# Optimization experiments

Measured on AMD Instinct MI355X. Metric: run time of the kernel, lower is better.

## Reference

```python
import jax, jax.numpy as jnp
import numpy as np

B, M, H = 4, 128, 1024      # docs, padded mentions per doc, LUKE-large hidden
NH, L = 16, 1024            # attention heads, seq_len
E = 64                      # padded entities per doc
R = 512                     # entity pairs per doc
EMB, BS, NC = 768, 64, 97   # embed_size, block_size, num_class


def setup_inputs() -> dict:
    key = jax.random.key(0)
    ks = jax.random.split(key, 12)
    inp = {
        "seq_lhs": jax.random.normal(ks[0], (B, L, H), jnp.float32),
        "ent_lhs": jax.random.normal(ks[1], (B, M, H), jnp.float32),
        "ent_to_seq_attn": jax.random.uniform(ks[2], (B, NH, M, L), jnp.float32),
        "entity_id_labels": jax.random.randint(ks[3], (B, M), 0, E),
        "hts": jax.random.randint(ks[4], (B, R, 2), 0, E),
        "Wh": jax.random.normal(ks[5], (2 * H, EMB), jnp.float32) * 0.02,
        "bh": jax.random.normal(ks[6], (EMB,), jnp.float32) * 0.02,
        "Wt": jax.random.normal(ks[7], (2 * H, EMB), jnp.float32) * 0.02,
        "bt": jax.random.normal(ks[8], (EMB,), jnp.float32) * 0.02,
        "Wb": jax.random.normal(ks[9], (EMB * BS, NC), jnp.float32) * 0.02,
        "bb": jax.random.normal(ks[10], (NC,), jnp.float32) * 0.02,
    }
    return inp


def reference(seq_lhs, ent_lhs, ent_to_seq_attn, entity_id_labels, hts,
              Wh, bh, Wt, bt, Wb, bb):
    # ---- mention -> entity pooling (segment logsumexp / segment mean) ----
    # global segment id per mention: doc_i * E + entity_label
    ids = (jnp.arange(B)[:, None] * E + entity_id_labels).reshape(-1)  # [B*M]
    m = ent_lhs.reshape(B * M, H)

    seg_max = jax.ops.segment_max(m, ids, num_segments=B * E)          # [B*E, H]
    seg_max = jnp.where(jnp.isfinite(seg_max), seg_max, 0.0)           # empty -> 0
    sumexp = jax.ops.segment_sum(jnp.exp(m - seg_max[ids]), ids, num_segments=B * E)
    cnt = jax.ops.segment_sum(jnp.ones((B * M,), m.dtype), ids, num_segments=B * E)  # [B*E]
    lse = seg_max + jnp.log(jnp.maximum(sumexp, 1e-30))
    ent_embeds = jnp.where(cnt[:, None] > 0, lse, 0.0).reshape(B, E, H)

    # mean of entity-to-seq attention over mentions of each entity
    a = ent_to_seq_attn.transpose(0, 2, 1, 3).reshape(B * M, NH, L)
    a_sum = jax.ops.segment_sum(a, ids, num_segments=B * E)            # [B*E, NH, L]
    ent_attn = (a_sum / jnp.maximum(cnt, 1.0)[:, None, None]).reshape(B, E, NH, L)

    # ---- gather head/tail entities for each pair ----
    h_idx, t_idx = hts[..., 0], hts[..., 1]                            # [B, R]
    hs = jnp.take_along_axis(ent_embeds, h_idx[..., None], axis=1)     # [B, R, H]
    ts = jnp.take_along_axis(ent_embeds, t_idx[..., None], axis=1)
    h_attn = jnp.take_along_axis(ent_attn, h_idx[..., None, None], axis=1)  # [B, R, NH, L]
    t_attn = jnp.take_along_axis(ent_attn, t_idx[..., None, None], axis=1)

    # ---- attn-weighted relation-context embedding ----
    ht_attn = (h_attn * t_attn).mean(axis=2)                           # [B, R, L]
    ht_attn = ht_attn / (ht_attn.sum(-1, keepdims=True) + 1e-5)
    rel = jnp.einsum('bld,brl->brd', seq_lhs, ht_attn)                 # [B, R, H]

    # ---- extractors + block bilinear classifier ----
    hs = jnp.tanh(jnp.concatenate([hs, rel], -1) @ Wh + bh)            # [B, R, EMB]
    ts = jnp.tanh(jnp.concatenate([ts, rel], -1) @ Wt + bt)
    N, K = B * R, EMB // BS
    b1 = hs.reshape(N, K, BS)
    b2 = ts.reshape(N, K, BS)
    bl = (b1[:, :, :, None] * b2[:, :, None, :]).reshape(N, EMB * BS)  # [N, 49152]
    class_logits = bl @ Wb + bb                                        # [N, NC]
    return class_logits
```

## Files before the change

### kernel.cpp

```cpp
#include <hip/hip_runtime.h>
#include <cmath>

#define B_ 4
#define M_ 128
#define H_ 1024
#define NH_ 16
#define L_ 1024
#define E_ 64
#define R_ 512
#define EMB_ 768
#define BS_ 64
#define NC_ 97
#define NPAIR_ (B_*R_)
#define LC_ 16

typedef _Float16 half8 __attribute__((ext_vector_type(8)));
typedef float f32x4 __attribute__((ext_vector_type(4)));

#define OFF_EAT    0
#define OFF_VH     2097152
#define OFF_PART   0
#define OFF_SEQT   3145728
#define OFF_G      3145728
#define OFF_RELH   5242880
#define OFF_WBT    6291456
#define OFF_ENTH   9437184
#define OFF_SV     9568256
#define OFF_WHT    9570304
#define OFF_WTT    10356736

__device__ __forceinline__ void gload_lds16(const void* g, void* l) {
    __builtin_amdgcn_global_load_lds(
        (const __attribute__((address_space(1))) unsigned int*)g,
        (__attribute__((address_space(3))) unsigned int*)l, 16, 0, 0);
}

__global__ __launch_bounds__(256) void k_ent_pool(const float* __restrict__ ent_lhs,
                                                  const int* __restrict__ labels,
                                                  _Float16* __restrict__ enth) {
    int blk = blockIdx.x;
    int b = blk >> 6, e = blk & 63;
    __shared__ int lbl[M_];
    int t = threadIdx.x;
    if (t < M_) lbl[t] = labels[b*M_ + t];
    __syncthreads();
    const float* src = ent_lhs + (size_t)b * M_ * H_;
    float mx[4], sm[4];
    #pragma unroll
    for (int j = 0; j < 4; ++j) { mx[j] = -INFINITY; sm[j] = 0.f; }
    int cnt = 0;
    for (int m = 0; m < M_; ++m) {
        if (lbl[m] != e) continue;
        ++cnt;
        const float* row = src + m * H_;
        #pragma unroll
        for (int j = 0; j < 4; ++j) {
            float x = row[t + j*256];
            if (x > mx[j]) { sm[j] = sm[j] * __expf(mx[j] - x) + 1.f; mx[j] = x; }
            else           { sm[j] += __expf(x - mx[j]); }
        }
    }
    _Float16* dst = enth + (size_t)blk * H_;
    #pragma unroll
    for (int j = 0; j < 4; ++j)
        dst[t + j*256] = (_Float16)((cnt > 0) ? (mx[j] + __logf(sm[j])) : 0.f);
}

__global__ __launch_bounds__(256) void k_ent_attn(const float* __restrict__ attn,
                                                  const int* __restrict__ labels,
                                                  _Float16* __restrict__ ea_t) {
    int blk = blockIdx.x;
    int b = blk >> 6, e = blk & 63;
    __shared__ int lbl[M_];
    int t = threadIdx.x;
    if (t < M_) lbl[t] = labels[b*M_ + t];
    __syncthreads();
    const float* src = attn + (size_t)b * NH_ * M_ * L_;
    float acc[16][4] = {};
    int cnt = 0;
    for (int m = 0; m < M_; ++m) {
        if (lbl[m] != e) continue;
        ++cnt;
        const float* mp = src + (size_t)m * L_ + t*4;
        #pragma unroll
        for (int nh = 0; nh < 16; ++nh) {
            float4 v = *(const float4*)(mp + (size_t)nh * M_ * L_);
            acc[nh][0] += v.x; acc[nh][1] += v.y; acc[nh][2] += v.z; acc[nh][3] += v.w;
        }
    }
    float inv = 1.f / fmaxf((float)cnt, 1.f);
    _Float16* dst = ea_t + (size_t)blk * L_ * 16;
    #pragma unroll
    for (int j = 0; j < 4; ++j) {
        int l = t*4 + j;
        half8 o0, o1;
        #pragma unroll
        for (int nh = 0; nh < 8; ++nh) { o0[nh] = (_Float16)(acc[nh][j]*inv); o1[nh] = (_Float16)(acc[nh+8][j]*inv); }
        *(half8*)(dst + (size_t)l*16)     = o0;
        *(half8*)(dst + (size_t)l*16 + 8) = o1;
    }
}

__global__ __launch_bounds__(256) void k_ht(const _Float16* __restrict__ ea_t,
                                            const int* __restrict__ hts,
                                            _Float16* __restrict__ vh) {
    int blk = blockIdx.x;
    int b = blk >> 6, lc = blk & 63;
    int l0 = lc * LC_;
    __shared__ _Float16 tile[64*256];
    int t = threadIdx.x;
    {
        int e = t >> 2, part = t & 3;
        const _Float16* src = ea_t + ((size_t)(b*64 + e)*L_ + l0) * 16;
        #pragma unroll
        for (int u = 0; u < 8; ++u) {
            int unit = part*8 + u;
            int l = unit >> 1, nhh = unit & 1;
            half8 v = *(const half8*)(src + l*16 + nhh*8);
            *(half8*)&tile[e*256 + ((l ^ (e & 15))*16) + nhh*8] = v;
        }
    }
    __syncthreads();
    const int* hp = hts + b * R_ * 2;
    #pragma unroll
    for (int pp = 0; pp < 2; ++pp) {
        int p = pp*256 + t;
        int he = hp[p*2], te = hp[p*2 + 1];
        const _Float16* ha = &tile[he*256];
        const _Float16* ta = &tile[te*256];
        float accl[LC_];
        #pragma unroll
        for (int l = 0; l < LC_; ++l) {
            half8 h0 = *(const half8*)&ha[((l ^ (he & 15))*16)];
            half8 h1 = *(const half8*)&ha[((l ^ (he & 15))*16) + 8];
            half8 t0 = *(const half8*)&ta[((l ^ (te & 15))*16)];
            half8 t1 = *(const half8*)&ta[((l ^ (te & 15))*16) + 8];
            float s = 0.f;
            #pragma unroll
            for (int q = 0; q < 8; ++q)
                s += (float)h0[q]*(float)t0[q] + (float)h1[q]*(float)t1[q];
            accl[l] = s;
        }
        half8 o0, o1;
        #pragma unroll
        for (int q = 0; q < 8; ++q) { o0[q] = (_Float16)accl[q]; o1[q] = (_Float16)accl[q+8]; }
        _Float16* dst = vh + (size_t)(b*R_ + p)*L_ + l0;
        *(half8*)dst = o0;
        *(half8*)(dst + 8) = o1;
    }
}

__global__ __launch_bounds__(256) void k_rowsum(const _Float16* __restrict__ vh,
                                                float* __restrict__ s) {
    int row = blockIdx.x*4 + (threadIdx.x >> 6);
    int lane = threadIdx.x & 63;
    const _Float16* r = vh + (size_t)row * L_;
    float acc = 0.f;
    #pragma unroll
    for (int u = 0; u < 2; ++u) {
        half8 v = *(const half8*)(r + (lane + u*64)*8);
        #pragma unroll
        for (int q = 0; q < 8; ++q) acc += (float)v[q];
    }
    #pragma unroll
    for (int off = 32; off > 0; off >>= 1) acc += __shfl_down(acc, off);
    if (lane == 0) s[row] = acc;
}

__global__ __launch_bounds__(256) void k_prep_seqt(const float* __restrict__ seq,
                                                   _Float16* __restrict__ seqT) {
    int l0 = blockIdx.x*64, d0 = blockIdx.y*64, b = blockIdx.z;
    __shared__ _Float16 sl[64*72];
    int t = threadIdx.x;
    int lr = t >> 4, dc = (t & 15)*4;
    #pragma unroll
    for (int u = 0; u < 4; ++u) {
        int l = lr + u*16;
        float4 v = *(const float4*)(seq + ((size_t)(b*L_ + l0 + l))*H_ + d0 + dc);
        sl[l*72 + dc+0] = (_Float16)v.x; sl[l*72 + dc+1] = (_Float16)v.y;
        sl[l*72 + dc+2] = (_Float16)v.z; sl[l*72 + dc+3] = (_Float16)v.w;
    }
    __syncthreads();
    int d = t >> 2, lo = (t & 3)*16;
    half8 o0, o1;
    #pragma unroll
    for (int q = 0; q < 8; ++q) { o0[q] = sl[(lo+q)*72 + d]; o1[q] = sl[(lo+8+q)*72 + d]; }
    _Float16* dst = seqT + ((size_t)(b*H_ + d0 + d))*L_ + l0 + lo;
    *(half8*)dst = o0;
    *(half8*)(dst + 8) = o1;
}

__global__ __launch_bounds__(256) void k_prep_wt(const float* __restrict__ W,
                                                 _Float16* __restrict__ WT) {
    int k0 = blockIdx.x * 64;
    int d0 = blockIdx.y * 64;
    __shared__ float s[64*65];
    int t = threadIdx.x;
    #pragma unroll
    for (int u = 0; u < 16; ++u) {
        int idx = t + u*256; int rr = idx >> 6, cc = idx & 63;
        s[rr*65 + cc] = W[(size_t)(k0+rr)*EMB_ + d0 + cc];
    }
    __syncthreads();
    #pragma unroll
    for (int u = 0; u < 16; ++u) {
        int idx = t + u*256; int dd = idx >> 6, kk = idx & 63;
        WT[(size_t)(d0+dd)*2048 + k0 + kk] = (_Float16)s[kk*65 + dd];
    }
}

__global__ __launch_bounds__(256) void k_prep_wbt(const float* __restrict__ Wb,
                                                  _Float16* __restrict__ Wbt) {
    int kbi = blockIdx.x;
    __shared__ float s[64*97];
    int t = threadIdx.x;
    size_t gbase = (size_t)kbi * 64 * NC_;
    #pragma unroll
    for (int u = 0; u < 25; ++u) {
        int idx = t + u*256;
        if (idx < 64*NC_) s[idx] = Wb[gbase + idx];
    }
    __syncthreads();
    _Float16* dst = Wbt + (size_t)kbi * 8192;
    #pragma unroll
    for (int u = 0; u < 32; ++u) {
        int idx = t + u*256;
        int c = idx >> 6, j = idx & 63;
        float v = (c < NC_) ? s[j*NC_ + c] : 0.f;
        dst[idx] = (_Float16)v;
    }
}

__global__ __launch_bounds__(256) void k_relmm(const _Float16* __restrict__ vh,
                                               const _Float16* __restrict__ seqT,
                                               const float* __restrict__ sv,
                                               _Float16* __restrict__ relh) {
    const int nt = blockIdx.x;
    const int mt = blockIdx.y;
    const int b  = mt >> 2;
    __shared__ _Float16 As[2][128*64];
    __shared__ _Float16 Bs[2][64*64];
    const int t = threadIdx.x;
    const int w = t >> 6, lane = t & 63;
    const int r = lane & 15, g = lane >> 4;
    const int wm = w >> 1, wn = w & 1;
    const int srow = lane >> 3, scol = ((lane & 7) ^ srow) * 8;

    const _Float16* Ab = vh + (size_t)mt*128*1024;
    const _Float16* Bb = seqT + ((size_t)b*1024 + nt*64)*1024;

    #pragma unroll
    for (int cc = 0; cc < 6; ++cc) {
        int c = w*6 + cc;
        if (c < 16) gload_lds16(Ab + (size_t)(c*8 + srow)*1024 + scol, &As[0][c*512]);
        else        gload_lds16(Bb + (size_t)((c-16)*8 + srow)*1024 + scol, &Bs[0][(c-16)*512]);
    }
    f32x4 acc[4][2] = {};
    __syncthreads();

    for (int k = 0; k < 16; ++k) {
        const int cur = k & 1;
        if (k < 15) {
            const int k0 = (k+1)*64;
            #pragma unroll
            for (int cc = 0; cc < 6; ++cc) {
                int c = w*6 + cc;
                if (c < 16) gload_lds16(Ab + (size_t)(c*8 + srow)*1024 + k0 + scol, &As[cur^1][c*512]);
                else        gload_lds16(Bb + (size_t)((c-16)*8 + srow)*1024 + k0 + scol, &Bs[cur^1][(c-16)*512]);
            }
        }
        half8 aF[4][2], bF[2][2];
        #pragma unroll
        for (int mf = 0; mf < 4; ++mf) {
            int row = wm*64 + mf*16 + r;
            aF[mf][0] = *(const half8*)&As[cur][row*64 + ((g ^ (r&7))*8)];
            aF[mf][1] = *(const half8*)&As[cur][row*64 + (((4+g) ^ (r&7))*8)];
        }
        #pragma unroll
        for (int nf = 0; nf < 2; ++nf) {
            int row = wn*32 + nf*16 + r;
            bF[nf][0] = *(const half8*)&Bs[cur][row*64 + ((g ^ (r&7))*8)];
            bF[nf][1] = *(const half8*)&Bs[cur][row*64 + (((4+g) ^ (r&7))*8)];
        }
        #pragma unroll
        for (int mf = 0; mf < 4; ++mf)
            #pragma unroll
            for (int nf = 0; nf < 2; ++nf) {
                acc[mf][nf] = __builtin_amdgcn_mfma_f32_16x16x32_f16(aF[mf][0], bF[nf][0], acc[mf][nf], 0, 0, 0);
                acc[mf][nf] = __builtin_amdgcn_mfma_f32_16x16x32_f16(aF[mf][1], bF[nf][1], acc[mf][nf], 0, 0, 0);
            }
        __syncthreads();
    }
    #pragma unroll
    for (int mf = 0; mf < 4; ++mf) {
        int nb = mt*128 + wm*64 + mf*16 + g*4;
        float invs[4];
        #pragma unroll
        for (int q = 0; q < 4; ++q) invs[q] = 1.f / (sv[nb + q] + 1.6e-4f);
        #pragma unroll
        for (int nf = 0; nf < 2; ++nf) {
            int d = nt*64 + wn*32 + nf*16 + r;
            #pragma unroll
            for (int q = 0; q < 4; ++q)
                relh[(size_t)(nb + q)*1024 + d] = (_Float16)(acc[mf][nf][q] * invs[q]);
        }
    }
}

__global__ __launch_bounds__(256) void k_bigmm(const _Float16* __restrict__ relh,
                                               const _Float16* __restrict__ enth,
                                               const _Float16* __restrict__ WhT,
                                               const _Float16* __restrict__ WtT,
                                               _Float16* __restrict__ G) {
    const int nt = blockIdx.x;
    const int mt = blockIdx.y;
    __shared__ _Float16 As[2][128*64];
    __shared__ _Float16 Bs[2][128*64];
    const int t = threadIdx.x;
    const int w = t >> 6, lane = t & 63;
    const int r = lane & 15, g = lane >> 4;
    const int wm = w >> 1, wn = w & 1;
    const int srow = lane >> 3, scol = ((lane & 7) ^ srow) * 8;

    const _Float16* Ab = (mt < 16) ? (relh + (size_t)mt*128*1024)
                                   : (enth + (size_t)(mt-16)*128*1024);
    const int koff = (mt < 16) ? 1024 : 0;
    const _Float16* Bb = ((nt < 6) ? (WhT + (size_t)nt*128*2048)
                                   : (WtT + (size_t)(nt-6)*128*2048)) + koff;

    #pragma unroll
    for (int cc = 0; cc < 4; ++cc) {
        int c = w*4 + cc;
        gload_lds16(Ab + (size_t)(c*8 + srow)*1024 + scol, &As[0][c*512]);
        gload_lds16(Bb + (size_t)(c*8 + srow)*2048 + scol, &Bs[0][c*512]);
    }
    f32x4 acc[4][4] = {};
    __syncthreads();

    for (int k = 0; k < 16; ++k) {
        const int cur = k & 1;
        if (k < 15) {
            const int k0 = (k+1)*64;
            #pragma unroll
            for (int cc = 0; cc < 4; ++cc) {
                int c = w*4 + cc;
                gload_lds16(Ab + (size_t)(c*8 + srow)*1024 + k0 + scol, &As[cur^1][c*512]);
                gload_lds16(Bb + (size_t)(c*8 + srow)*2048 + k0 + scol, &Bs[cur^1][c*512]);
            }
        }
        half8 aF[4][2], bF[4][2];
        #pragma unroll
        for (int mf = 0; mf < 4; ++mf) {
            int row = wm*64 + mf*16 + r;
            aF[mf][0] = *(const half8*)&As[cur][row*64 + ((g ^ (r&7))*8)];
            aF[mf][1] = *(const half8*)&As[cur][row*64 + (((4+g) ^ (r&7))*8)];
        }
        #pragma unroll
        for (int nf = 0; nf < 4; ++nf) {
            int row = wn*64 + nf*16 + r;
            bF[nf][0] = *(const half8*)&Bs[cur][row*64 + ((g ^ (r&7))*8)];
            bF[nf][1] = *(const half8*)&Bs[cur][row*64 + (((4+g) ^ (r&7))*8)];
        }
        #pragma unroll
        for (int mf = 0; mf < 4; ++mf)
            #pragma unroll
            for (int nf = 0; nf < 4; ++nf) {
                acc[mf][nf] = __builtin_amdgcn_mfma_f32_16x16x32_f16(aF[mf][0], bF[nf][0], acc[mf][nf], 0, 0, 0);
                acc[mf][nf] = __builtin_amdgcn_mfma_f32_16x16x32_f16(aF[mf][1], bF[nf][1], acc[mf][nf], 0, 0, 0);
            }
        __syncthreads();
    }
    #pragma unroll
    for (int mf = 0; mf < 4; ++mf) {
        int nrow = mt*128 + wm*64 + mf*16 + g*4;
        #pragma unroll
        for (int nf = 0; nf < 4; ++nf) {
            int v = nt*128 + wn*64 + nf*16 + r;
            #pragma unroll
            for (int q = 0; q < 4; ++q)
                G[(size_t)(nrow + q)*1536 + v] = (_Float16)acc[mf][nf][q];
        }
    }
}

__global__ __launch_bounds__(192) void k_combine(const _Float16* __restrict__ G,
                                                 const int* __restrict__ hts,
                                                 const float* __restrict__ bh,
                                                 const float* __restrict__ bt,
                                                 _Float16* __restrict__ hsf,
                                                 _Float16* __restrict__ tsf) {
    int n = blockIdx.x;
    int b = n >> 9;
    int t = threadIdx.x;
    int side = t / 96, u = t % 96;
    int d0 = u*8;
    int idx = hts[n*2 + side];
    const _Float16* grel = G + (size_t)n*1536 + side*768 + d0;
    const _Float16* gent = G + (size_t)(2048 + b*64 + idx)*1536 + side*768 + d0;
    const float* bias = side ? bt : bh;
    half8 a = *(const half8*)grel;
    half8 e = *(const half8*)gent;
    half8 o;
    #pragma unroll
    for (int q = 0; q < 8; ++q)
        o[q] = (_Float16)tanhf((float)a[q] + (float)e[q] + bias[d0+q]);
    _Float16* dst = (side ? tsf : hsf) + (size_t)n*EMB_ + d0;
    *(half8*)dst = o;
}

__global__ __launch_bounds__(256) void k_cls_mfma(const _Float16* __restrict__ hsf,
                                                  const _Float16* __restrict__ tsf,
                                                  const _Float16* __restrict__ Wbt,
                                                  float* __restrict__ partial) {
    const int kb = blockIdx.x;
    const int n0 = blockIdx.y * 128;
    const int t = threadIdx.x;
    const int w = t >> 6, lane = t & 63;
    const int r = lane & 15, g = lane >> 4;
    __shared__ _Float16 hs_s[128*72];

    {
        int n = t & 127, hh = t >> 7;
        const _Float16* src = &hsf[(size_t)(n0+n)*EMB_ + kb*64 + hh*32];
        #pragma unroll
        for (int u = 0; u < 4; ++u)
            *(half8*)&hs_s[n*72 + hh*32 + u*8] = *(const half8*)(src + u*8);
    }
    half8 tsF[8][2];
    #pragma unroll
    for (int nf = 0; nf < 8; ++nf) {
        const _Float16* tp = &tsf[(size_t)(n0 + nf*16 + r)*EMB_ + kb*64];
        tsF[nf][0] = *(const half8*)(tp + g*8);
        tsF[nf][1] = *(const half8*)(tp + 32 + g*8);
    }
    __syncthreads();

    const _Float16* wb = Wbt + (size_t)(kb*64) * 8192;
    f32x4 acc[8][2] = {};

    #pragma unroll 2
    for (int i = 0; i < 64; ++i) {
        const _Float16* ws_ = wb + (size_t)i * 8192;
        half8 b00, b01, b10, b11;
        {
            const _Float16* bp0 = ws_ + (size_t)(w*32 + r)*64;
            const _Float16* bp1 = ws_ + (size_t)(w*32 + 16 + r)*64;
            b00 = *(const half8*)(bp0 + g*8);
            b01 = *(const half8*)(bp0 + 32 + g*8);
            b10 = *(const half8*)(bp1 + g*8);
            b11 = *(const half8*)(bp1 + 32 + g*8);
        }
        #pragma unroll
        for (int nf = 0; nf < 8; ++nf) {
            _Float16 h = hs_s[(nf*16 + r)*72 + i];
            half8 a0, a1;
            #pragma unroll
            for (int e = 0; e < 8; ++e) { a0[e] = tsF[nf][0][e] * h; a1[e] = tsF[nf][1][e] * h; }
            acc[nf][0] = __builtin_amdgcn_mfma_f32_16x16x32_f16(a0, b00, acc[nf][0], 0, 0, 0);
            acc[nf][0] = __builtin_amdgcn_mfma_f32_16x16x32_f16(a1, b01, acc[nf][0], 0, 0, 0);
            acc[nf][1] = __builtin_amdgcn_mfma_f32_16x16x32_f16(a0, b10, acc[nf][1], 0, 0, 0);
            acc[nf][1] = __builtin_amdgcn_mfma_f32_16x16x32_f16(a1, b11, acc[nf][1], 0, 0, 0);
        }
    }
    float* pdst = partial + (size_t)kb * 2048 * 128;
    #pragma unroll
    for (int nf = 0; nf < 8; ++nf) {
        #pragma unroll
        for (int cl = 0; cl < 2; ++cl) {
            int c = w*32 + cl*16 + r;
            #pragma unroll
            for (int q = 0; q < 4; ++q)
                pdst[(size_t)(n0 + nf*16 + g*4 + q)*128 + c] = acc[nf][cl][q];
        }
    }
}

__global__ __launch_bounds__(256) void k_reduce(const float* __restrict__ partial,
                                                const float* __restrict__ bb,
                                                float* __restrict__ out) {
    int idx = blockIdx.x*256 + threadIdx.x;
    if (idx >= NPAIR_*NC_) return;
    int n = idx / NC_, c = idx - n*NC_;
    float s = bb[c];
    #pragma unroll
    for (int kb = 0; kb < 12; ++kb)
        s += partial[((size_t)kb*2048 + n)*128 + c];
    out[idx] = s;
}

extern "C" void kernel_launch(void* const* d_in, const int* in_sizes, int n_in,
                              void* d_out, int out_size, void* d_ws, size_t ws_size,
                              hipStream_t stream) {
    (void)in_sizes; (void)n_in; (void)out_size; (void)ws_size;
    const float* seq  = (const float*)d_in[0];
    const float* ent  = (const float*)d_in[1];
    const float* attn = (const float*)d_in[2];
    const int*   lbl  = (const int*)d_in[3];
    const int*   hts  = (const int*)d_in[4];
    const float* Wh   = (const float*)d_in[5];
    const float* bh   = (const float*)d_in[6];
    const float* Wt   = (const float*)d_in[7];
    const float* bt   = (const float*)d_in[8];
    const float* Wb   = (const float*)d_in[9];
    const float* bb   = (const float*)d_in[10];
    float* out = (float*)d_out;
    float* ws  = (float*)d_ws;

    _Float16* ea_t = (_Float16*)(ws + OFF_EAT);
    _Float16* vh   = (_Float16*)(ws + OFF_VH);
    float*    part = ws + OFF_PART;
    _Float16* seqT = (_Float16*)(ws + OFF_SEQT);
    _Float16* G    = (_Float16*)(ws + OFF_G);
    _Float16* relh = (_Float16*)(ws + OFF_RELH);
    _Float16* Wbt  = (_Float16*)(ws + OFF_WBT);
    _Float16* enth = (_Float16*)(ws + OFF_ENTH);
    float*    sv   = ws + OFF_SV;
    _Float16* WhT  = (_Float16*)(ws + OFF_WHT);
    _Float16* WtT  = (_Float16*)(ws + OFF_WTT);
    _Float16* hsf  = (_Float16*)(ws + OFF_WHT);
    _Float16* tsf  = (_Float16*)(ws + OFF_WTT);

    k_prep_seqt<<<dim3(16, 16, 4), 256, 0, stream>>>(seq, seqT);
    k_prep_wt<<<dim3(32, 12), 256, 0, stream>>>(Wh, WhT);
    k_prep_wt<<<dim3(32, 12), 256, 0, stream>>>(Wt, WtT);
    k_prep_wbt<<<768, 256, 0, stream>>>(Wb, Wbt);
    k_ent_pool<<<B_*E_, 256, 0, stream>>>(ent, lbl, enth);
    k_ent_attn<<<B_*E_, 256, 0, stream>>>(attn, lbl, ea_t);
    k_ht<<<B_*64, 256, 0, stream>>>(ea_t, hts, vh);
    k_rowsum<<<NPAIR_/4, 256, 0, stream>>>(vh, sv);
    k_relmm<<<dim3(16, 16), 256, 0, stream>>>(vh, seqT, sv, relh);
    k_bigmm<<<dim3(12, 18), 256, 0, stream>>>(relh, enth, WhT, WtT, G);
    k_combine<<<NPAIR_, 192, 0, stream>>>(G, hts, bh, bt, hsf, tsf);
    k_cls_mfma<<<dim3(12, 16), 256, 0, stream>>>(hsf, tsf, Wbt, part);
    k_reduce<<<(NPAIR_*NC_ + 255)/256, 256, 0, stream>>>(part, bb, out);
}
```

Baseline: 281.2 us.

## Fuse prep kernels into one launch and fold rowsum into k_ht via atomics

```diff
diff --git a/kernel.cpp b/kernel.cpp
--- a/kernel.cpp
+++ b/kernel.cpp
@@ -35,75 +35,145 @@
         (__attribute__((address_space(3))) unsigned int*)l, 16, 0, 0);
 }
 
-__global__ __launch_bounds__(256) void k_ent_pool(const float* __restrict__ ent_lhs,
-                                                  const int* __restrict__ labels,
-                                                  _Float16* __restrict__ enth) {
-    int blk = blockIdx.x;
-    int b = blk >> 6, e = blk & 63;
-    __shared__ int lbl[M_];
-    int t = threadIdx.x;
-    if (t < M_) lbl[t] = labels[b*M_ + t];
-    __syncthreads();
-    const float* src = ent_lhs + (size_t)b * M_ * H_;
-    float mx[4], sm[4];
-    #pragma unroll
-    for (int j = 0; j < 4; ++j) { mx[j] = -INFINITY; sm[j] = 0.f; }
-    int cnt = 0;
-    for (int m = 0; m < M_; ++m) {
-        if (lbl[m] != e) continue;
-        ++cnt;
-        const float* row = src + m * H_;
+__global__ __launch_bounds__(256) void k_prep_fused(const float* __restrict__ seq,
+                                                    const float* __restrict__ Wh,
+                                                    const float* __restrict__ Wt,
+                                                    const float* __restrict__ Wb,
+                                                    const float* __restrict__ ent_lhs,
+                                                    const float* __restrict__ attn,
+                                                    const int* __restrict__ labels,
+                                                    _Float16* __restrict__ seqT,
+                                                    _Float16* __restrict__ WhT,
+                                                    _Float16* __restrict__ WtT,
+                                                    _Float16* __restrict__ Wbt,
+                                                    _Float16* __restrict__ enth,
+                                                    _Float16* __restrict__ ea_t,
+                                                    float* __restrict__ sv) {
+    __shared__ __align__(16) char smem_raw[24832];
+    const int bid = blockIdx.x;
+    const int t = threadIdx.x;
+
+    if (bid < 1024) {
+        _Float16* sl = (_Float16*)smem_raw;
+        int l0 = (bid & 15)*64, d0 = ((bid >> 4) & 15)*64, b = bid >> 8;
+        int lr = t >> 4, dc = (t & 15)*4;
+        #pragma unroll
+        for (int u = 0; u < 4; ++u) {
+            int l = lr + u*16;
+            float4 v = *(const float4*)(seq + ((size_t)(b*L_ + l0 + l))*H_ + d0 + dc);
+            sl[l*72 + dc+0] = (_Float16)v.x; sl[l*72 + dc+1] = (_Float16)v.y;
+            sl[l*72 + dc+2] = (_Float16)v.z; sl[l*72 + dc+3] = (_Float16)v.w;
+        }
+        __syncthreads();
+        int d = t >> 2, lo = (t & 3)*16;
+        half8 o0, o1;
+        #pragma unroll
+        for (int q = 0; q < 8; ++q) { o0[q] = sl[(lo+q)*72 + d]; o1[q] = sl[(lo+8+q)*72 + d]; }
+        _Float16* dst = seqT + ((size_t)(b*H_ + d0 + d))*L_ + l0 + lo;
+        *(half8*)dst = o0;
+        *(half8*)(dst + 8) = o1;
+    } else if (bid < 1792) {
+        const bool isH = bid < 1408;
+        const float* W = isH ? Wh : Wt;
+        _Float16* WT = isH ? WhT : WtT;
+        int i = bid - (isH ? 1024 : 1408);
+        int k0 = (i & 31)*64, d0 = (i >> 5)*64;
+        float* s = (float*)smem_raw;
+        #pragma unroll
+        for (int u = 0; u < 16; ++u) {
+            int idx = t + u*256; int rr = idx >> 6, cc = idx & 63;
+            s[rr*65 + cc] = W[(size_t)(k0+rr)*EMB_ + d0 + cc];
+        }
+        __syncthreads();
+        #pragma unroll
+        for (int u = 0; u < 16; ++u) {
+            int idx = t + u*256; int dd = idx >> 6, kk = idx & 63;
+            WT[(size_t)(d0+dd)*2048 + k0 + kk] = (_Float16)s[kk*65 + dd];
+        }
+    } else if (bid < 2560) {
+        int kbi = bid - 1792;
+        float* s = (float*)smem_raw;
+        size_t gbase = (size_t)kbi * 64 * NC_;
+        #pragma unroll
+        for (int u = 0; u < 25; ++u) {
+            int idx = t + u*256;
+            if (idx < 64*NC_) s[idx] = Wb[gbase + idx];
+        }
+        __syncthreads();
+        _Float16* dst = Wbt + (size_t)kbi * 8192;
+        #pragma unroll
+        for (int u = 0; u < 32; ++u) {
+            int idx = t + u*256;
+            int c = idx >> 6, j = idx & 63;
+            float v = (c < NC_) ? s[j*NC_ + c] : 0.f;
+            dst[idx] = (_Float16)v;
+        }
+    } else if (bid < 2816) {
+        int blk = bid - 2560;
+        int b = blk >> 6, e = blk & 63;
+        int* lbl = (int*)smem_raw;
+        if (t < M_) lbl[t] = labels[b*M_ + t];
+        __syncthreads();
+        const float* src = ent_lhs + (size_t)b * M_ * H_;
+        float mx[4], sm[4];
+        #pragma unroll
+        for (int j = 0; j < 4; ++j) { mx[j] = -INFINITY; sm[j] = 0.f; }
+        int cnt = 0;
+        for (int m = 0; m < M_; ++m) {
+            if (lbl[m] != e) continue;
+            ++cnt;
+            const float* row = src + m * H_;
+            #pragma unroll
+            for (int j = 0; j < 4; ++j) {
+                float x = row[t + j*256];
+                if (x > mx[j]) { sm[j] = sm[j] * __expf(mx[j] - x) + 1.f; mx[j] = x; }
+                else           { sm[j] += __expf(x - mx[j]); }
+            }
+        }
+        _Float16* dst = enth + (size_t)blk * H_;
+        #pragma unroll
+        for (int j = 0; j < 4; ++j)
+            dst[t + j*256] = (_Float16)((cnt > 0) ? (mx[j] + __logf(sm[j])) : 0.f);
+    } else if (bid < 3072) {
+        int blk = bid - 2816;
+        int b = blk >> 6, e = blk & 63;
+        int* lbl = (int*)smem_raw;
+        if (t < M_) lbl[t] = labels[b*M_ + t];
+        __syncthreads();
+        const float* src = attn + (size_t)b * NH_ * M_ * L_;
+        float acc[16][4] = {};
+        int cnt = 0;
+        for (int m = 0; m < M_; ++m) {
+            if (lbl[m] != e) continue;
+            ++cnt;
+            const float* mp = src + (size_t)m * L_ + t*4;
+            #pragma unroll
+            for (int nh = 0; nh < 16; ++nh) {
+                float4 v = *(const float4*)(mp + (size_t)nh * M_ * L_);
+                acc[nh][0] += v.x; acc[nh][1] += v.y; acc[nh][2] += v.z; acc[nh][3] += v.w;
+            }
+        }
+        float inv = 1.f / fmaxf((float)cnt, 1.f);
+        _Float16* dst = ea_t + (size_t)blk * L_ * 16;
         #pragma unroll
         for (int j = 0; j < 4; ++j) {
-            float x = row[t + j*256];
-            if (x > mx[j]) { sm[j] = sm[j] * __expf(mx[j] - x) + 1.f; mx[j] = x; }
-            else           { sm[j] += __expf(x - mx[j]); }
-        }
-    }
-    _Float16* dst = enth + (size_t)blk * H_;
-    #pragma unroll
-    for (int j = 0; j < 4; ++j)
-        dst[t + j*256] = (_Float16)((cnt > 0) ? (mx[j] + __logf(sm[j])) : 0.f);
-}
-
-__global__ __launch_bounds__(256) void k_ent_attn(const float* __restrict__ attn,
-                                                  const int* __restrict__ labels,
-                                                  _Float16* __restrict__ ea_t) {
-    int blk = blockIdx.x;
-    int b = blk >> 6, e = blk & 63;
-    __shared__ int lbl[M_];
-    int t = threadIdx.x;
-    if (t < M_) lbl[t] = labels[b*M_ + t];
-    __syncthreads();
-    const float* src = attn + (size_t)b * NH_ * M_ * L_;
-    float acc[16][4] = {};
-    int cnt = 0;
-    for (int m = 0; m < M_; ++m) {
-        if (lbl[m] != e) continue;
-        ++cnt;
-        const float* mp = src + (size_t)m * L_ + t*4;
-        #pragma unroll
-        for (int nh = 0; nh < 16; ++nh) {
-            float4 v = *(const float4*)(mp + (size_t)nh * M_ * L_);
-            acc[nh][0] += v.x; acc[nh][1] += v.y; acc[nh][2] += v.z; acc[nh][3] += v.w;
-        }
-    }
-    float inv = 1.f / fmaxf((float)cnt, 1.f);
-    _Float16* dst = ea_t + (size_t)blk * L_ * 16;
-    #pragma unroll
-    for (int j = 0; j < 4; ++j) {
-        int l = t*4 + j;
-        half8 o0, o1;
-        #pragma unroll
-        for (int nh = 0; nh < 8; ++nh) { o0[nh] = (_Float16)(acc[nh][j]*inv); o1[nh] = (_Float16)(acc[nh+8][j]*inv); }
-        *(half8*)(dst + (size_t)l*16)     = o0;
-        *(half8*)(dst + (size_t)l*16 + 8) = o1;
+            int l = t*4 + j;
+            half8 o0, o1;
+            #pragma unroll
+            for (int nh = 0; nh < 8; ++nh) { o0[nh] = (_Float16)(acc[nh][j]*inv); o1[nh] = (_Float16)(acc[nh+8][j]*inv); }
+            *(half8*)(dst + (size_t)l*16)     = o0;
+            *(half8*)(dst + (size_t)l*16 + 8) = o1;
+        }
+    } else {
+        int idx = (bid - 3072)*256 + t;
+        if (idx < NPAIR_) sv[idx] = 0.f;
     }
 }
 
 __global__ __launch_bounds__(256) void k_ht(const _Float16* __restrict__ ea_t,
                                             const int* __restrict__ hts,
-                                            _Float16* __restrict__ vh) {
+                                            _Float16* __restrict__ vh,
+                                            float* __restrict__ sv) {
     int blk = blockIdx.x;
     int b = blk >> 6, lc = blk & 63;
     int l0 = lc * LC_;
@@ -129,6 +199,7 @@
         const _Float16* ha = &tile[he*256];
         const _Float16* ta = &tile[te*256];
         float accl[LC_];
+        float psum = 0.f;
         #pragma unroll
         for (int l = 0; l < LC_; ++l) {
             half8 h0 = *(const half8*)&ha[((l ^ (he & 15))*16)];
@@ -140,6 +211,7 @@
             for (int q = 0; q < 8; ++q)
                 s += (float)h0[q]*(float)t0[q] + (float)h1[q]*(float)t1[q];
             accl[l] = s;
+            psum += s;
         }
         half8 o0, o1;
         #pragma unroll
@@ -147,87 +219,7 @@
         _Float16* dst = vh + (size_t)(b*R_ + p)*L_ + l0;
         *(half8*)dst = o0;
         *(half8*)(dst + 8) = o1;
-    }
-}
-
-__global__ __launch_bounds__(256) void k_rowsum(const _Float16* __restrict__ vh,
-                                                float* __restrict__ s) {
-    int row = blockIdx.x*4 + (threadIdx.x >> 6);
-    int lane = threadIdx.x & 63;
-    const _Float16* r = vh + (size_t)row * L_;
-    float acc = 0.f;
-    #pragma unroll
-    for (int u = 0; u < 2; ++u) {
-        half8 v = *(const half8*)(r + (lane + u*64)*8);
-        #pragma unroll
-        for (int q = 0; q < 8; ++q) acc += (float)v[q];
-    }
-    #pragma unroll
-    for (int off = 32; off > 0; off >>= 1) acc += __shfl_down(acc, off);
-    if (lane == 0) s[row] = acc;
-}
-
-__global__ __launch_bounds__(256) void k_prep_seqt(const float* __restrict__ seq,
-                                                   _Float16* __restrict__ seqT) {
-    int l0 = blockIdx.x*64, d0 = blockIdx.y*64, b = blockIdx.z;
-    __shared__ _Float16 sl[64*72];
-    int t = threadIdx.x;
-    int lr = t >> 4, dc = (t & 15)*4;
-    #pragma unroll
-    for (int u = 0; u < 4; ++u) {
-        int l = lr + u*16;
-        float4 v = *(const float4*)(seq + ((size_t)(b*L_ + l0 + l))*H_ + d0 + dc);
-        sl[l*72 + dc+0] = (_Float16)v.x; sl[l*72 + dc+1] = (_Float16)v.y;
-        sl[l*72 + dc+2] = (_Float16)v.z; sl[l*72 + dc+3] = (_Float16)v.w;
-    }
-    __syncthreads();
-    int d = t >> 2, lo = (t & 3)*16;
-    half8 o0, o1;
-    #pragma unroll
-    for (int q = 0; q < 8; ++q) { o0[q] = sl[(lo+q)*72 + d]; o1[q] = sl[(lo+8+q)*72 + d]; }
-    _Float16* dst = seqT + ((size_t)(b*H_ + d0 + d))*L_ + l0 + lo;
-    *(half8*)dst = o0;
-    *(half8*)(dst + 8) = o1;
-}
-
-__global__ __launch_bounds__(256) void k_prep_wt(const float* __restrict__ W,
-                                                 _Float16* __restrict__ WT) {
-    int k0 = blockIdx.x * 64;
-    int d0 = blockIdx.y * 64;
-    __shared__ float s[64*65];
-    int t = threadIdx.x;
-    #pragma unroll
-    for (int u = 0; u < 16; ++u) {
-        int idx = t + u*256; int rr = idx >> 6, cc = idx & 63;
-        s[rr*65 + cc] = W[(size_t)(k0+rr)*EMB_ + d0 + cc];
-    }
-    __syncthreads();
-    #pragma unroll
-    for (int u = 0; u < 16; ++u) {
-        int idx = t + u*256; int dd = idx >> 6, kk = idx & 63;
-        WT[(size_t)(d0+dd)*2048 + k0 + kk] = (_Float16)s[kk*65 + dd];
-    }
-}
-
-__global__ __launch_bounds__(256) void k_prep_wbt(const float* __restrict__ Wb,
-                                                  _Float16* __restrict__ Wbt) {
-    int kbi = blockIdx.x;
-    __shared__ float s[64*97];
-    int t = threadIdx.x;
-    size_t gbase = (size_t)kbi * 64 * NC_;
-    #pragma unroll
-    for (int u = 0; u < 25; ++u) {
-        int idx = t + u*256;
-        if (idx < 64*NC_) s[idx] = Wb[gbase + idx];
-    }
-    __syncthreads();
-    _Float16* dst = Wbt + (size_t)kbi * 8192;
-    #pragma unroll
-    for (int u = 0; u < 32; ++u) {
-        int idx = t + u*256;
-        int c = idx >> 6, j = idx & 63;
-        float v = (c < NC_) ? s[j*NC_ + c] : 0.f;
-        dst[idx] = (_Float16)v;
+        atomicAdd(&sv[b*R_ + p], psum);
     }
 }
 
@@ -520,14 +512,9 @@
     _Float16* hsf  = (_Float16*)(ws + OFF_WHT);
     _Float16* tsf  = (_Float16*)(ws + OFF_WTT);
 
-    k_prep_seqt<<<dim3(16, 16, 4), 256, 0, stream>>>(seq, seqT);
-    k_prep_wt<<<dim3(32, 12), 256, 0, stream>>>(Wh, WhT);
-    k_prep_wt<<<dim3(32, 12), 256, 0, stream>>>(Wt, WtT);
-    k_prep_wbt<<<768, 256, 0, stream>>>(Wb, Wbt);
-    k_ent_pool<<<B_*E_, 256, 0, stream>>>(ent, lbl, enth);
-    k_ent_attn<<<B_*E_, 256, 0, stream>>>(attn, lbl, ea_t);
-    k_ht<<<B_*64, 256, 0, stream>>>(ea_t, hts, vh);
-    k_rowsum<<<NPAIR_/4, 256, 0, stream>>>(vh, sv);
+    k_prep_fused<<<3080, 256, 0, stream>>>(seq, Wh, Wt, Wb, ent, attn, lbl,
+                                           seqT, WhT, WtT, Wbt, enth, ea_t, sv);
+    k_ht<<<B_*64, 256, 0, stream>>>(ea_t, hts, vh, sv);
     k_relmm<<<dim3(16, 16), 256, 0, stream>>>(vh, seqT, sv, relh);
     k_bigmm<<<dim3(12, 18), 256, 0, stream>>>(relh, enth, WhT, WtT, G);
     k_combine<<<NPAIR_, 192, 0, stream>>>(G, hts, bh, bt, hsf, tsf);
```

Result: faster. 253.8 us (-9.7%).
